# Performance work log

Hardware: AMD Instinct MI355X
Metric: run time of the kernel (lower is better)

## Reference

```python
import jax, jax.numpy as jnp
import numpy as np

K = 32        # top-k per row (init kwarg k)
TAU = 1.0     # gumbel temperature (init kwarg tau)
EPS = 1e-08
NEG_INF = -1e9


def setup_inputs() -> dict:
    key = jax.random.key(0)
    k1, k2 = jax.random.split(key)
    N = 8192
    logits = jax.random.normal(k1, (N, N), dtype=jnp.float32)
    u = jax.random.uniform(k2, (N, N), dtype=jnp.float32)
    return {"logits": logits, "u": u}


def reference(logits, u):
    # Gumbel noise: -log(-log(U + eps) + eps), matching torch.rand_like usage
    gumbel = -jnp.log(-jnp.log(u + EPS) + EPS)
    perturbed = (logits + gumbel) / TAU
    # Row-wise top-k indices on perturbed logits
    _, top_idx = jax.lax.top_k(perturbed, K)          # [N, K]
    # Scatter a hard 0/1 mask at the selected indices
    N = logits.shape[0]
    rows = jnp.arange(N)[:, None]                      # [N, 1]
    mask = jnp.zeros_like(logits).at[rows, top_idx].set(1.0)
    # Masked softmax over the ORIGINAL logits (noise only selects)
    masked_logits = logits * mask + (1.0 - mask) * NEG_INF
    adjacency = jax.nn.softmax(masked_logits, axis=-1)
    return adjacency
```

## Files before the change

### kernel.cpp

```cpp
#include <hip/hip_runtime.h>
#include <cstdint>

#define ROW_N 8192
#define TPB   256
#define CAP   512

__device__ __forceinline__ unsigned int fkey(float p) {
  unsigned int b = __float_as_uint(p);
  return (b & 0x80000000u) ? ~b : (b | 0x80000000u);
}
__device__ __forceinline__ float fkey_inv(unsigned int t) {
  unsigned int b = (t & 0x80000000u) ? (t & 0x7fffffffu) : ~t;
  return __uint_as_float(b);
}

__device__ __forceinline__ unsigned int akey(float lg, float uu) {
  float l2u = __log2f(uu + 1e-8f);
  float w   = fmaf(l2u, -0.6931471805599453f, 1e-8f);
  float p2  = fmaf(lg, 1.4426950408889634f, -__log2f(w));
  p2 = (w < 1e-5f) ? 3.0e38f : p2;
  return fkey(p2);
}

__device__ __forceinline__ uint64_t shfl_xor_u64(uint64_t v, int m) {
  unsigned int lo = (unsigned int)v, hi = (unsigned int)(v >> 32);
  lo = __shfl_xor(lo, m, 64);
  hi = __shfl_xor(hi, m, 64);
  return ((uint64_t)hi << 32) | lo;
}
__device__ __forceinline__ uint64_t wave_max_u64(uint64_t v) {
#pragma unroll
  for (int s = 32; s >= 1; s >>= 1) {
    uint64_t o = shfl_xor_u64(v, s);
    v = (o > v) ? o : v;
  }
  return v;
}

struct alignas(16) u64x2 { uint64_t a, b; };

__global__ __launch_bounds__(TPB, 4) void gumbel_topk_kernel(
    const float* __restrict__ logits, const float* __restrict__ u,
    float* __restrict__ out) {
  const int row  = blockIdx.x;
  const int tid  = threadIdx.x;
  const int lane = tid & 63;
  const int wave = tid >> 6;

  __shared__ unsigned int s_cnt, s_t;
  __shared__ alignas(16) unsigned int s_gmax[64];
  __shared__ unsigned int s_idx[CAP];
  __shared__ alignas(16) uint64_t s_comp[CAP + 2];
  __shared__ float        s_lg[CAP];
  __shared__ float        s_red[8];

  if (tid == 0) { s_cnt = 0; s_t = 0xFFFFFFFFu; }

  const float4* L4 = reinterpret_cast<const float4*>(logits) + (size_t)row * (ROW_N / 4);
  const float4* U4 = reinterpret_cast<const float4*>(u)      + (size_t)row * (ROW_N / 4);
  float4*       O4 = reinterpret_cast<float4*>(out)          + (size_t)row * (ROW_N / 4);

  float4 lv[8], uv[8];
#pragma unroll
  for (int j = 0; j < 8; ++j) {
    lv[j] = L4[j * TPB + tid];
    uv[j] = U4[j * TPB + tid];
  }

  {
    float4 z = make_float4(0.f, 0.f, 0.f, 0.f);
#pragma unroll
    for (int j = 0; j < 8; ++j) O4[j * TPB + tid] = z;
  }

  unsigned int k[32];
  unsigned int M = 0;
#pragma unroll
  for (int j = 0; j < 8; ++j) {
    k[j * 4 + 0] = akey(lv[j].x, uv[j].x);
    k[j * 4 + 1] = akey(lv[j].y, uv[j].y);
    k[j * 4 + 2] = akey(lv[j].z, uv[j].z);
    k[j * 4 + 3] = akey(lv[j].w, uv[j].w);
    M = max(M, max(max(k[j * 4 + 0], k[j * 4 + 1]), max(k[j * 4 + 2], k[j * 4 + 3])));
  }

  {
    unsigned int g = max(M, (unsigned int)__shfl_xor(M, 1, 64));
    g = max(g, (unsigned int)__shfl_xor(g, 2, 64));
    if ((tid & 3) == 0) s_gmax[tid >> 2] = g;
  }
  __syncthreads();
  if (tid < 64) {
    unsigned int mine = s_gmax[tid];
    unsigned int cnt = 0;
    const uint4* gm4 = reinterpret_cast<const uint4*>(s_gmax);
#pragma unroll
    for (int i = 0; i < 16; ++i) {
      uint4 v = gm4[i];
      cnt += (v.x > mine) + (v.y > mine) + (v.z > mine) + (v.w > mine);
    }
    if (cnt < 32) atomicMin(&s_t, mine);
  }
  __syncthreads();
  const unsigned int tm = fkey(fkey_inv(s_t) - 0.25f);

#pragma unroll
  for (int j = 0; j < 8; ++j) {
#pragma unroll
    for (int c = 0; c < 4; ++c) {
      if (k[j * 4 + c] >= tm) {
        unsigned int slot = atomicAdd(&s_cnt, 1u);
        if (slot < CAP)
          s_idx[slot] = (unsigned int)(j * TPB + tid) * 4u + (unsigned int)c;
      }
    }
  }
  __syncthreads();
  unsigned int C = s_cnt;

  if (C > CAP) {
#pragma unroll 1
    for (int it = 0; it < 32; ++it) {
      uint64_t lm = 0;
#pragma unroll
      for (int i = 0; i < 32; ++i) {
        unsigned int idx = (unsigned int)((i >> 2) * TPB + tid) * 4u + (unsigned int)(i & 3);
        uint64_t comp = ((uint64_t)k[i] << 13) | (uint64_t)(8191u - idx);
        if (k[i] != 0u && comp > lm) lm = comp;
      }
      uint64_t wm = wave_max_u64(lm);
      if (lm == wm) {
#pragma unroll
        for (int i = 0; i < 32; ++i) {
          unsigned int idx = (unsigned int)((i >> 2) * TPB + tid) * 4u + (unsigned int)(i & 3);
          uint64_t comp = ((uint64_t)k[i] << 13) | (uint64_t)(8191u - idx);
          if (comp == wm) k[i] = 0u;
        }
      }
      if (lane == 0) s_idx[wave * 32 + it] = 8191u - (unsigned int)(wm & 8191u);
    }
    __syncthreads();
    C = 128;
  }

  const float* Lrow = logits + (size_t)row * ROW_N;
  const float* Urow = u      + (size_t)row * ROW_N;
#pragma unroll 1
  for (unsigned int vi = tid; vi < C; vi += TPB) {
    unsigned int idx = s_idx[vi];
    float lg = Lrow[idx];
    float uu = Urow[idx];
    float p  = lg - logf(-logf(uu + 1e-8f) + 1e-8f);
    s_comp[vi] = ((uint64_t)fkey(p) << 13) | (uint64_t)(8191u - idx);
    s_lg[vi]   = lg;
  }
  if (tid == 0) s_comp[C] = 0;
  __syncthreads();

  float m_local = -3.4e38f;
  unsigned int sel = 0;
  float lgs[2];
  unsigned int ids[2];
  const unsigned int CP = (C + 1u) >> 1;
#pragma unroll
  for (int s = 0; s < 2; ++s) {
    unsigned int vi = tid + s * TPB;
    lgs[s] = 0.f; ids[s] = 0;
    if (vi < C) {
      uint64_t mine = s_comp[vi];
      unsigned int cnt = 0;
      const u64x2* c2 = reinterpret_cast<const u64x2*>(s_comp);
#pragma unroll 1
      for (unsigned int i = 0; i < CP; ++i) {
        u64x2 v = c2[i];
        cnt += (v.a > mine) ? 1u : 0u;
        cnt += (v.b > mine) ? 1u : 0u;
      }
      if (cnt < 32) {
        sel |= (1u << s);
        lgs[s] = s_lg[vi];
        ids[s] = s_idx[vi];
        m_local = fmaxf(m_local, lgs[s]);
      }
    }
  }

  float m = m_local;
#pragma unroll
  for (int s = 32; s >= 1; s >>= 1) m = fmaxf(m, __shfl_xor(m, s, 64));
  if (lane == 0) s_red[wave] = m;
  __syncthreads();
  m = fmaxf(fmaxf(s_red[0], s_red[1]), fmaxf(s_red[2], s_red[3]));

  float e0 = (sel & 1u) ? expf(lgs[0] - m) : 0.f;
  float e1 = (sel & 2u) ? expf(lgs[1] - m) : 0.f;
  float sum = e0 + e1;
#pragma unroll
  for (int s = 32; s >= 1; s >>= 1) sum += __shfl_xor(sum, s, 64);
  if (lane == 0) s_red[4 + wave] = sum;
  __syncthreads();
  sum = (s_red[4] + s_red[5]) + (s_red[6] + s_red[7]);

  float* Orow = out + (size_t)row * ROW_N;
  if (sel & 1u) Orow[ids[0]] = e0 / sum;
  if (sel & 2u) Orow[ids[1]] = e1 / sum;
}

extern "C" void kernel_launch(void* const* d_in, const int* in_sizes, int n_in,
                              void* d_out, int out_size, void* d_ws, size_t ws_size,
                              hipStream_t stream) {
  const float* logits = (const float*)d_in[0];
  const float* u      = (const float*)d_in[1];
  float*       out    = (float*)d_out;
  int rows = in_sizes[0] / ROW_N;
  gumbel_topk_kernel<<<dim3(rows), dim3(TPB), 0, stream>>>(logits, u, out);
}
```

Measured before the change: 599.6 us.

## Stage rows into LDS via async global_load_lds and reuse for candidate gather

The row's logits and uniform noise now go into a 64KB shared-memory buffer through the async global-to-LDS load builtin. Each chunk is consumed under its own staged vmcnt wait, so key computation can overlap with the loads still in flight. The candidate re-evaluation reads from LDS instead of doing scattered global reads, and the buffer is reused for the comparison arrays. The cost is heavy LDS use, with launch bounds dropped to 2 blocks per CU, which may reduce occupancy and latency hiding.

```diff
diff --git a/kernel.cpp b/kernel.cpp
--- a/kernel.cpp
+++ b/kernel.cpp
@@ -39,7 +39,26 @@
 
 struct alignas(16) u64x2 { uint64_t a, b; };
 
-__global__ __launch_bounds__(TPB, 4) void gumbel_topk_kernel(
+typedef const __attribute__((address_space(1))) unsigned int* gas_u32;
+typedef __attribute__((address_space(3)))       unsigned int* las_u32;
+
+#define STAGE16(gp, lp) \
+  __builtin_amdgcn_global_load_lds((gas_u32)(gp), (las_u32)(lp), 16, 0, 0)
+
+#define CONSUME(c, N)                                                          \
+  {                                                                            \
+    asm volatile("s_waitcnt vmcnt(" #N ")" ::: "memory");                      \
+    __builtin_amdgcn_sched_barrier(0);                                         \
+    float4 lv = *reinterpret_cast<const float4*>(&s_L[wbase + (c)*256 + loff]);\
+    float4 uv = *reinterpret_cast<const float4*>(&s_U[wbase + (c)*256 + loff]);\
+    k[(c)*4 + 0] = akey(lv.x, uv.x);                                           \
+    k[(c)*4 + 1] = akey(lv.y, uv.y);                                           \
+    k[(c)*4 + 2] = akey(lv.z, uv.z);                                           \
+    k[(c)*4 + 3] = akey(lv.w, uv.w);                                           \
+    M = max(M, max(max(k[(c)*4+0], k[(c)*4+1]), max(k[(c)*4+2], k[(c)*4+3]))); \
+  }
+
+__global__ __launch_bounds__(TPB, 2) void gumbel_topk_kernel(
     const float* __restrict__ logits, const float* __restrict__ u,
     float* __restrict__ out) {
   const int row  = blockIdx.x;
@@ -47,41 +66,39 @@
   const int lane = tid & 63;
   const int wave = tid >> 6;
 
+  __shared__ alignas(16) float s_stage[2 * ROW_N];
+  __shared__ unsigned int s_idx[CAP];
+  __shared__ alignas(16) unsigned int s_gmax[64];
   __shared__ unsigned int s_cnt, s_t;
-  __shared__ alignas(16) unsigned int s_gmax[64];
-  __shared__ unsigned int s_idx[CAP];
-  __shared__ alignas(16) uint64_t s_comp[CAP + 2];
-  __shared__ float        s_lg[CAP];
-  __shared__ float        s_red[8];
+  __shared__ float s_red[8];
+
+  float* s_L = s_stage;
+  float* s_U = s_stage + ROW_N;
 
   if (tid == 0) { s_cnt = 0; s_t = 0xFFFFFFFFu; }
 
-  const float4* L4 = reinterpret_cast<const float4*>(logits) + (size_t)row * (ROW_N / 4);
-  const float4* U4 = reinterpret_cast<const float4*>(u)      + (size_t)row * (ROW_N / 4);
-  float4*       O4 = reinterpret_cast<float4*>(out)          + (size_t)row * (ROW_N / 4);
-
-  float4 lv[8], uv[8];
-#pragma unroll
-  for (int j = 0; j < 8; ++j) {
-    lv[j] = L4[j * TPB + tid];
-    uv[j] = U4[j * TPB + tid];
-  }
+  const float* Lrow = logits + (size_t)row * ROW_N;
+  const float* Urow = u      + (size_t)row * ROW_N;
+  float4*      O4   = reinterpret_cast<float4*>(out) + (size_t)row * (ROW_N / 4);
+
+  const int wbase = wave * 2048;
+  const int loff  = lane * 4;
+
+#pragma unroll
+  for (int i = 0; i < 8; ++i) {
+    STAGE16(Lrow + wbase + i * 256 + loff, &s_L[wbase + i * 256]);
+    STAGE16(Urow + wbase + i * 256 + loff, &s_U[wbase + i * 256]);
+  }
+
+  unsigned int k[32];
+  unsigned int M = 0;
+  CONSUME(0, 14) CONSUME(1, 12) CONSUME(2, 10) CONSUME(3, 8)
+  CONSUME(4, 6)  CONSUME(5, 4)  CONSUME(6, 2)  CONSUME(7, 0)
 
   {
     float4 z = make_float4(0.f, 0.f, 0.f, 0.f);
 #pragma unroll
     for (int j = 0; j < 8; ++j) O4[j * TPB + tid] = z;
-  }
-
-  unsigned int k[32];
-  unsigned int M = 0;
-#pragma unroll
-  for (int j = 0; j < 8; ++j) {
-    k[j * 4 + 0] = akey(lv[j].x, uv[j].x);
-    k[j * 4 + 1] = akey(lv[j].y, uv[j].y);
-    k[j * 4 + 2] = akey(lv[j].z, uv[j].z);
-    k[j * 4 + 3] = akey(lv[j].w, uv[j].w);
-    M = max(M, max(max(k[j * 4 + 0], k[j * 4 + 1]), max(k[j * 4 + 2], k[j * 4 + 3])));
   }
 
   {
@@ -104,6 +121,7 @@
   __syncthreads();
   const unsigned int tm = fkey(fkey_inv(s_t) - 0.25f);
 
+  const unsigned int tbase = (unsigned int)(wbase + loff);
 #pragma unroll
   for (int j = 0; j < 8; ++j) {
 #pragma unroll
@@ -111,7 +129,7 @@
       if (k[j * 4 + c] >= tm) {
         unsigned int slot = atomicAdd(&s_cnt, 1u);
         if (slot < CAP)
-          s_idx[slot] = (unsigned int)(j * TPB + tid) * 4u + (unsigned int)c;
+          s_idx[slot] = tbase + (unsigned int)(j * 256 + c);
       }
     }
   }
@@ -124,7 +142,7 @@
       uint64_t lm = 0;
 #pragma unroll
       for (int i = 0; i < 32; ++i) {
-        unsigned int idx = (unsigned int)((i >> 2) * TPB + tid) * 4u + (unsigned int)(i & 3);
+        unsigned int idx = tbase + (unsigned int)((i >> 2) * 256 + (i & 3));
         uint64_t comp = ((uint64_t)k[i] << 13) | (uint64_t)(8191u - idx);
         if (k[i] != 0u && comp > lm) lm = comp;
       }
@@ -132,7 +150,7 @@
       if (lm == wm) {
 #pragma unroll
         for (int i = 0; i < 32; ++i) {
-          unsigned int idx = (unsigned int)((i >> 2) * TPB + tid) * 4u + (unsigned int)(i & 3);
+          unsigned int idx = tbase + (unsigned int)((i >> 2) * 256 + (i & 3));
           uint64_t comp = ((uint64_t)k[i] << 13) | (uint64_t)(8191u - idx);
           if (comp == wm) k[i] = 0u;
         }
@@ -143,16 +161,31 @@
     C = 128;
   }
 
-  const float* Lrow = logits + (size_t)row * ROW_N;
-  const float* Urow = u      + (size_t)row * ROW_N;
-#pragma unroll 1
-  for (unsigned int vi = tid; vi < C; vi += TPB) {
-    unsigned int idx = s_idx[vi];
-    float lg = Lrow[idx];
-    float uu = Urow[idx];
-    float p  = lg - logf(-logf(uu + 1e-8f) + 1e-8f);
-    s_comp[vi] = ((uint64_t)fkey(p) << 13) | (uint64_t)(8191u - idx);
-    s_lg[vi]   = lg;
+  uint64_t compv[2];
+  float    lgvv[2];
+  unsigned int idxs[2];
+#pragma unroll
+  for (int s = 0; s < 2; ++s) {
+    unsigned int vi = (unsigned int)tid + (unsigned int)s * TPB;
+    compv[s] = 0; lgvv[s] = 0.f; idxs[s] = 0;
+    if (vi < C) {
+      unsigned int idx = s_idx[vi];
+      idxs[s] = idx;
+      float lg = s_L[idx];
+      float uu = s_U[idx];
+      float p  = lg - logf(-logf(uu + 1e-8f) + 1e-8f);
+      compv[s] = ((uint64_t)fkey(p) << 13) | (uint64_t)(8191u - idx);
+      lgvv[s]  = lg;
+    }
+  }
+  __syncthreads();
+
+  uint64_t* s_comp = reinterpret_cast<uint64_t*>(s_stage);
+  float*    s_lg   = s_stage + 2 * (CAP + 2);
+#pragma unroll
+  for (int s = 0; s < 2; ++s) {
+    unsigned int vi = (unsigned int)tid + (unsigned int)s * TPB;
+    if (vi < C) { s_comp[vi] = compv[s]; s_lg[vi] = lgvv[s]; }
   }
   if (tid == 0) s_comp[C] = 0;
   __syncthreads();
@@ -160,14 +193,13 @@
   float m_local = -3.4e38f;
   unsigned int sel = 0;
   float lgs[2];
-  unsigned int ids[2];
   const unsigned int CP = (C + 1u) >> 1;
 #pragma unroll
   for (int s = 0; s < 2; ++s) {
-    unsigned int vi = tid + s * TPB;
-    lgs[s] = 0.f; ids[s] = 0;
+    unsigned int vi = (unsigned int)tid + (unsigned int)s * TPB;
+    lgs[s] = 0.f;
     if (vi < C) {
-      uint64_t mine = s_comp[vi];
+      uint64_t mine = compv[s];
       unsigned int cnt = 0;
       const u64x2* c2 = reinterpret_cast<const u64x2*>(s_comp);
 #pragma unroll 1
@@ -178,8 +210,7 @@
       }
       if (cnt < 32) {
         sel |= (1u << s);
-        lgs[s] = s_lg[vi];
-        ids[s] = s_idx[vi];
+        lgs[s] = lgvv[s];
         m_local = fmaxf(m_local, lgs[s]);
       }
     }
@@ -202,8 +233,8 @@
   sum = (s_red[4] + s_red[5]) + (s_red[6] + s_red[7]);
 
   float* Orow = out + (size_t)row * ROW_N;
-  if (sel & 1u) Orow[ids[0]] = e0 / sum;
-  if (sel & 2u) Orow[ids[1]] = e1 / sum;
+  if (sel & 1u) Orow[idxs[0]] = e0 / sum;
+  if (sel & 2u) Orow[idxs[1]] = e1 / sum;
 }
 
 extern "C" void kernel_launch(void* const* d_in, const int* in_sizes, int n_in,
```

After: 617.9 us. 1.03x slower.
